# Optimization experiments

Hardware: AMD Instinct MI355X
Metric: run time of the kernel (lower is better)

## Reference

```python
import jax, jax.numpy as jnp
import numpy as np
from functools import partial

B, S, D_IN, H = 8, 2048, 1024, 1024
V = 50257
NUM_CODEWORDS, EMB_DIM = 256, 16
NUM_NEURONS, TOP_K = 64, 16  # top_k = sparsity(0.25) * 64
TILE_ROWS = 16
NUM_TILES = H // TILE_ROWS  # 64 -> decoder out_features = 1024
FREQS = (1.0, 2.0, 4.0)
MAX_LEN = 1024


def setup_inputs() -> dict:
    key = jax.random.key(0)
    ks = jax.random.split(key, 16)
    s = 0.02
    return {
        "inputs": jax.random.normal(ks[0], (B, S, D_IN), jnp.float32),
        "Wt": jax.random.normal(ks[1], (H, D_IN), jnp.float32) * s,
        "bt": jnp.zeros((H,), jnp.float32),
        "Wq": jax.random.normal(ks[2], (H, H), jnp.float32) * s,
        "bq": jnp.zeros((H,), jnp.float32),
        "Wk": jax.random.normal(ks[3], (H, H), jnp.float32) * s,
        "bk": jnp.zeros((H,), jnp.float32),
        "Wv": jax.random.normal(ks[4], (H, H), jnp.float32) * s,
        "bv": jnp.zeros((H,), jnp.float32),
        "Wo": jax.random.normal(ks[5], (D_IN, H), jnp.float32) * s,
        "bo": jnp.zeros((D_IN,), jnp.float32),
        "codebook": jax.random.normal(ks[6], (NUM_CODEWORDS, EMB_DIM), jnp.float32) * s,
        "instructions": jax.random.randint(ks[7], (NUM_TILES * TILE_ROWS, D_IN // EMB_DIM), 0, NUM_CODEWORDS),
        "W_lm": jax.random.normal(ks[8], (V, NUM_TILES * TILE_ROWS), jnp.float32) * s,
        "b_lm": jnp.zeros((V,), jnp.float32),
    }


def _positional_bias(seq_len):
    # AttentionBasisSynthesizer: sin/cos atoms at freqs (1,2,4), gains=1, shifts=0
    ang = 2.0 * jnp.pi * jnp.arange(seq_len, dtype=jnp.float32) / MAX_LEN
    bias = jnp.zeros((seq_len,), jnp.float32)
    for f in FREQS:
        bias = bias + jnp.sin(f * ang) + jnp.cos(f * ang)
    return bias  # [S]


def _forward(inputs, Wt, bt, Wq, bq, Wk, bk, Wv, bv, Wo, bo, codebook, instructions, W_lm, b_lm):
    tokens = inputs @ Wt.T + bt                       # [B,S,H]
    q = tokens @ Wq.T + bq
    k = tokens @ Wk.T + bk
    v = tokens @ Wv.T + bv
    # per-step KV-cache loop == causal attention over prefix; vectorize
    scores = jnp.einsum("bqh,bkh->bqk", q, k) / jnp.sqrt(jnp.float32(H))
    scores = scores + _positional_bias(S)[None, None, :]
    i = jnp.arange(S)
    causal = i[:, None] >= i[None, :]                 # [S,S]
    scores = jnp.where(causal[None], scores, -jnp.inf)
    attn = jnp.einsum("bqk,bkh->bqh", jax.nn.softmax(scores, axis=-1), v)  # [B,S,H]
    # sparse routing: group into NUM_NEURONS neurons, keep top-k by L2 norm,
    # softmax weights over kept neurons, straight-through combine with dense path
    g = attn.reshape(B, S, NUM_NEURONS, H // NUM_NEURONS)
    sc = jnp.sqrt(jnp.sum(g * g, axis=-1))            # [B,S,N]
    vals, idx = jax.lax.top_k(sc, TOP_K)              # [B,S,K]
    w = jax.nn.softmax(vals, axis=-1)
    onehot = jax.nn.one_hot(idx, NUM_NEURONS, dtype=attn.dtype)  # [B,S,K,N]
    wfull = jnp.einsum("bsk,bskn->bsn", w, onehot)    # [B,S,N]
    combined = (g * wfull[..., None]).reshape(B, S, H)
    combined = combined + (attn - jax.lax.stop_gradient(attn))  # straight-through
    dec_in = combined @ Wo.T + bo                     # [B,S,D_IN]
    x = jnp.mean(dec_in, axis=1)                      # [B,D_IN]
    # DemopackDecoder: weight rows assembled from codebook via instruction indices
    W_dec = codebook[instructions].reshape(NUM_TILES * TILE_ROWS, D_IN)
    hidden = x @ W_dec.T                              # [B, 1024]
    return hidden @ W_lm.T + b_lm                     # [B, V]


def reference(inputs, Wt, bt, Wq, bq, Wk, bk, Wv, bv, Wo, bo, codebook, instructions, W_lm, b_lm):
    return _forward(inputs, Wt, bt, Wq, bq, Wk, bk, Wv, bv, Wo, bo, codebook, instructions, W_lm, b_lm)
```

## Files before the change

### kernel.cpp

```cpp
#include <hip/hip_runtime.h>
#include <cstdint>
#include <cstddef>

#define B_   8
#define S_   2048
#define DIN_ 1024
#define H_   1024
#define V_   50257

typedef unsigned short ushort_t;
typedef __bf16 bf16x8 __attribute__((ext_vector_type(8)));
typedef float  f32x4  __attribute__((ext_vector_type(4)));

__device__ __forceinline__ ushort_t f2bf(float x) {
    unsigned u = __float_as_uint(x);
    u = (u + 0x7fffu + ((u >> 16) & 1u)) >> 16;
    return (ushort_t)u;
}

__device__ __forceinline__ void async16(const void* g, void* s) {
    __builtin_amdgcn_global_load_lds(
        (const __attribute__((address_space(1))) unsigned int*)g,
        (__attribute__((address_space(3))) unsigned int*)s, 16, 0, 0);
}

__device__ __forceinline__ float wredmax(float v) {
#pragma unroll
    for (int o = 32; o; o >>= 1) v = fmaxf(v, __shfl_xor(v, o));
    return v;
}
__device__ __forceinline__ float wredsum(float v) {
#pragma unroll
    for (int o = 32; o; o >>= 1) v += __shfl_xor(v, o);
    return v;
}

__global__ void f2bf_vec(const float* __restrict__ in, ushort_t* __restrict__ out, int n4) {
    int i = blockIdx.x * 256 + threadIdx.x;
    if (i >= n4) return;
    float4 f = ((const float4*)in)[i];
    ushort4 u;
    u.x = f2bf(f.x); u.y = f2bf(f.y); u.z = f2bf(f.z); u.w = f2bf(f.w);
    ((ushort4*)out)[i] = u;
}

__global__ void f2bf_w3(const float* __restrict__ Wq, const float* __restrict__ Wk,
                        const float* __restrict__ Wv, ushort_t* __restrict__ out) {
    int i = blockIdx.x * 256 + threadIdx.x;
    int w = i >> 18, off = i & 262143;
    const float* src = w == 0 ? Wq : (w == 1 ? Wk : Wv);
    float4 f = ((const float4*)src)[off];
    ushort4 u;
    u.x = f2bf(f.x); u.y = f2bf(f.y); u.z = f2bf(f.z); u.w = f2bf(f.w);
    ((ushort4*)(out + (size_t)w * 1048576))[off] = u;
}

__global__ void pos_bias_kernel(float* __restrict__ bias) {
    int k = blockIdx.x * 256 + threadIdx.x;
    if (k >= S_) return;
    float ang = 6.283185307179586f * (float)k / 1024.0f;
    float b = 0.f;
    b += sinf(1.f * ang) + cosf(1.f * ang);
    b += sinf(2.f * ang) + cosf(2.f * ang);
    b += sinf(4.f * ang) + cosf(4.f * ang);
    bias[k] = b;
}

__global__ __launch_bounds__(256)
void transpose_wt(const float* __restrict__ Wt, ushort_t* __restrict__ wtT) {
    __shared__ float t[64][65];
    int k0 = blockIdx.x * 64, i0 = blockIdx.y * 64;
    int tx = threadIdx.x & 63, ty = threadIdx.x >> 6;
#pragma unroll
    for (int j = 0; j < 16; j++) {
        int k = ty * 16 + j;
        t[k][tx] = Wt[(size_t)(k0 + k) * DIN_ + i0 + tx];
    }
    __syncthreads();
#pragma unroll
    for (int j = 0; j < 16; j++) {
        int i = ty * 16 + j;
        wtT[(size_t)(i0 + i) * H_ + k0 + tx] = f2bf(t[tx][i]);
    }
}

__global__ __launch_bounds__(256)
void bcomb_kernel(const float* __restrict__ Wq, const float* __restrict__ Wk,
                  const float* __restrict__ Wv, const float* __restrict__ bq,
                  const float* __restrict__ bk, const float* __restrict__ bv,
                  const float* __restrict__ bt, float* __restrict__ bcomb) {
    int wave = threadIdx.x >> 6, lane = threadIdx.x & 63;
    int j = blockIdx.x * 4 + wave;
    const float* W  = j < 1024 ? Wq : (j < 2048 ? Wk : Wv);
    const float* bb = j < 1024 ? bq : (j < 2048 ? bk : bv);
    int rowj = j & 1023;
    const float4* wr4 = (const float4*)(W + (size_t)rowj * 1024);
    const float4* bt4 = (const float4*)bt;
    float s = 0.f;
#pragma unroll
    for (int c = 0; c < 4; c++) {
        float4 w = wr4[c * 64 + lane];
        float4 b = bt4[c * 64 + lane];
        s += w.x * b.x + w.y * b.y + w.z * b.z + w.w * b.w;
    }
    s = wredsum(s);
    if (lane == 0) bcomb[j] = s + bb[rowj];
}

template <int OUT_BF16>
__global__ __launch_bounds__(256)
void gemm_bt(const ushort_t* __restrict__ A, int lda,
             const ushort_t* __restrict__ Bt, int ldb,
             void* __restrict__ Cv, int ldc, int K, const float* __restrict__ bias) {
    int bn = blockIdx.x, bm = blockIdx.y;
    __shared__ ushort_t As[128 * 32];
    __shared__ ushort_t Bs[128 * 32];
    int tid = threadIdx.x, wave = tid >> 6, lane = tid & 63;
    int wr = wave >> 1, wc = wave & 1;
    int nkt = K >> 5;
    int srow = lane >> 2, scol = (lane & 3) * 8;
    size_t arow0 = (size_t)bm * 128, brow0 = (size_t)bn * 128;
    f32x4 acc[4][4];
#pragma unroll
    for (int m = 0; m < 4; m++)
#pragma unroll
        for (int n = 0; n < 4; n++) acc[m][n] = f32x4{0.f, 0.f, 0.f, 0.f};
    for (int kt = 0; kt < nkt; ++kt) {
        int k0 = kt * 32;
#pragma unroll
        for (int i = 0; i < 2; i++) {
            int reg = wave * 2 + i;
            int row = reg * 16 + srow;
            async16(A + (arow0 + row) * (size_t)lda + k0 + scol, (ushort_t*)As + reg * 512);
            async16(Bt + (brow0 + row) * (size_t)ldb + k0 + scol, (ushort_t*)Bs + reg * 512);
        }
        __syncthreads();
        bf16x8 af[4], bfr[4];
#pragma unroll
        for (int m = 0; m < 4; m++)
            af[m] = *(const bf16x8*)&As[(wr * 64 + m * 16 + (lane & 15)) * 32 + (lane >> 4) * 8];
#pragma unroll
        for (int n = 0; n < 4; n++)
            bfr[n] = *(const bf16x8*)&Bs[(wc * 64 + n * 16 + (lane & 15)) * 32 + (lane >> 4) * 8];
#pragma unroll
        for (int m = 0; m < 4; m++)
#pragma unroll
            for (int n = 0; n < 4; n++)
                acc[m][n] = __builtin_amdgcn_mfma_f32_16x16x32_bf16(af[m], bfr[n], acc[m][n], 0, 0, 0);
        __syncthreads();
    }
    int rl = (lane >> 4) * 4, cl = lane & 15;
#pragma unroll
    for (int m = 0; m < 4; m++)
#pragma unroll
        for (int n = 0; n < 4; n++) {
            int col = bn * 128 + wc * 64 + n * 16 + cl;
            float badd = bias ? bias[col] : 0.f;
#pragma unroll
            for (int r = 0; r < 4; r++) {
                int row = bm * 128 + wr * 64 + m * 16 + rl + r;
                float v = acc[m][n][r] + badd;
                size_t off = (size_t)row * ldc + col;
                if (OUT_BF16) ((ushort_t*)Cv)[off] = f2bf(v);
                else          ((float*)Cv)[off] = v;
            }
        }
}

template <int OUT_BF16, int MODE>
__global__ __launch_bounds__(512, 2)
void gemm256(const ushort_t* __restrict__ A, size_t sAb, int lda,
             const ushort_t* __restrict__ Bt, size_t sBb, int ldb,
             void* __restrict__ Cv, size_t sCb, int ldc,
             int K, const float* __restrict__ bias, int nbn, int nwg,
             float* __restrict__ Cv2) {
    extern __shared__ char lds[];
    int bz = blockIdx.y;
    int bm, bn, koff = 0, nkt;
    void* Cuse = Cv;
    size_t sCuse = sCb;
    if (MODE == 2) {
        int x = blockIdx.x;
        if (x < 32) {
            bm = x >> 2; bn = x & 3;
            int km = (bm + 1) * 256; if (km > 1024) km = 1024;
            nkt = km >> 6;
        } else {
            int j = x - 32;
            bm = 7 - (j >> 2); bn = j & 3;
            koff = 1024;
            nkt = ((bm + 1) * 256 - 1024) >> 6;
            Cuse = Cv2;
            sCuse = (size_t)1024 * 1024;
        }
    } else {
        int orig = blockIdx.x;
        int qq = nwg >> 3, rr8 = nwg & 7;
        int xcd = orig & 7, bidx = orig >> 3;
        int wgid = (xcd < rr8 ? xcd * (qq + 1) : rr8 * (qq + 1) + (xcd - rr8) * qq) + bidx;
        if (MODE == 1) {
            int w = wgid;
            bm = 0;
            while ((bm + 1) * (bm + 2) / 2 <= w) bm++;
            bn = w - bm * (bm + 1) / 2;
        } else {
            bm = wgid / nbn; bn = wgid - bm * nbn;
        }
        nkt = K >> 6;
    }

    const ushort_t* Ab = A + (size_t)bz * sAb;
    const ushort_t* Bb = Bt + (size_t)bz * sBb;
    int tid = threadIdx.x, wave = tid >> 6, lane = tid & 63;
    int wr = wave >> 2, wc = wave & 3;

    int srow = wave * 8 + (lane >> 3);
    int sswz = ((lane & 7) ^ (lane >> 3)) * 8;
    const ushort_t* Ag = Ab + ((size_t)bm * 256 + srow) * (size_t)lda + sswz + koff;
    const ushort_t* Bg = Bb + ((size_t)bn * 256 + srow) * (size_t)ldb + sswz + koff;
    int sdst = wave * 1024;

    int fr = lane & 15, g = lane >> 4;
    int kx = (fr >> 2) & 1;
    int gsw = (g ^ (fr & 3)) * 16;
    int aoff = wr * 16384 + fr * 128 + gsw;
    int boff = 32768 + (wc >> 1) * 16384 + ((wc & 1) * 64 + fr) * 128 + gsw;
    int ks0 = kx << 6, ks1 = (kx ^ 1) << 6;

    f32x4 acc[8][4];
#pragma unroll
    for (int m = 0; m < 8; m++)
#pragma unroll
        for (int n = 0; n < 4; n++) acc[m][n] = f32x4{0.f, 0.f, 0.f, 0.f};

#define STG_A(t, h, bo)                                                        \
    do {                                                                       \
        async16(Ag + (size_t)((h) * 128) * lda + (t) * 64,                     \
                lds + (bo) + (h) * 16384 + sdst);                              \
        async16(Ag + (size_t)((h) * 128 + 64) * lda + (t) * 64,                \
                lds + (bo) + (h) * 16384 + 8192 + sdst);                       \
    } while (0)
#define STG_B(t, h, bo)                                                        \
    do {                                                                       \
        async16(Bg + (size_t)((h) * 128) * ldb + (t) * 64,                     \
                lds + (bo) + 32768 + (h) * 16384 + sdst);                      \
        async16(Bg + (size_t)((h) * 128 + 64) * ldb + (t) * 64,                \
                lds + (bo) + 32768 + (h) * 16384 + 8192 + sdst);               \
    } while (0)

    STG_A(0, 0, 0); STG_A(0, 1, 0); STG_B(0, 0, 0); STG_B(0, 1, 0);
    STG_A(1, 0, 65536); STG_A(1, 1, 65536); STG_B(1, 0, 65536); STG_B(1, 1, 65536);
    asm volatile("s_waitcnt vmcnt(8)" ::: "memory");
    __builtin_amdgcn_sched_barrier(0);
    __builtin_amdgcn_s_barrier();
    __builtin_amdgcn_sched_barrier(0);

    bf16x8 af03[4][2], af47[4][2], bf01[2][2], bf23[2][2];
#pragma unroll
    for (int mf = 0; mf < 4; mf++) {
        af03[mf][0] = *(const bf16x8*)(lds + aoff + mf * 2048 + ks0);
        af03[mf][1] = *(const bf16x8*)(lds + aoff + mf * 2048 + ks1);
    }
#pragma unroll
    for (int nf = 0; nf < 2; nf++) {
        bf01[nf][0] = *(const bf16x8*)(lds + boff + nf * 2048 + ks0);
        bf01[nf][1] = *(const bf16x8*)(lds + boff + nf * 2048 + ks1);
    }

    int bufo = 0;
    for (int t = 0; t < nkt; ++t, bufo ^= 65536) {
        int nb = bufo ^ 65536;
#pragma unroll
        for (int mf = 0; mf < 4; mf++) {
            af47[mf][0] = *(const bf16x8*)(lds + bufo + aoff + (mf + 4) * 2048 + ks0);
            af47[mf][1] = *(const bf16x8*)(lds + bufo + aoff + (mf + 4) * 2048 + ks1);
        }
#pragma unroll
        for (int nf = 0; nf < 2; nf++) {
            bf23[nf][0] = *(const bf16x8*)(lds + bufo + boff + (nf + 2) * 2048 + ks0);
            bf23[nf][1] = *(const bf16x8*)(lds + bufo + boff + (nf + 2) * 2048 + ks1);
        }
        __builtin_amdgcn_s_setprio(1);
#pragma unroll
        for (int mf = 0; mf < 4; mf++)
#pragma unroll
            for (int nf = 0; nf < 2; nf++) {
                acc[mf][nf] = __builtin_amdgcn_mfma_f32_16x16x32_bf16(af03[mf][0], bf01[nf][0], acc[mf][nf], 0, 0, 0);
                acc[mf][nf] = __builtin_amdgcn_mfma_f32_16x16x32_bf16(af03[mf][1], bf01[nf][1], acc[mf][nf], 0, 0, 0);
            }
        __builtin_amdgcn_s_setprio(0);
        __builtin_amdgcn_sched_barrier(0);
        asm volatile("s_waitcnt lgkmcnt(0)" ::: "memory");
        __builtin_amdgcn_sched_barrier(0);
        __builtin_amdgcn_s_barrier();
        __builtin_amdgcn_sched_barrier(0);

        __builtin_amdgcn_s_setprio(1);
#pragma unroll
        for (int mf = 0; mf < 4; mf++)
#pragma unroll
            for (int nf = 0; nf < 2; nf++) {
                acc[mf + 4][nf] = __builtin_amdgcn_mfma_f32_16x16x32_bf16(af47[mf][0], bf01[nf][0], acc[mf + 4][nf], 0, 0, 0);
                acc[mf + 4][nf] = __builtin_amdgcn_mfma_f32_16x16x32_bf16(af47[mf][1], bf01[nf][1], acc[mf + 4][nf], 0, 0, 0);
            }
        __builtin_amdgcn_s_setprio(0);
        __builtin_amdgcn_sched_barrier(0);
        __builtin_amdgcn_s_barrier();
        __builtin_amdgcn_sched_barrier(0);

        if (t + 2 < nkt) STG_A(t + 2, 0, bufo);
        __builtin_amdgcn_s_setprio(1);
#pragma unroll
        for (int mf = 0; mf < 4; mf++)
#pragma unroll
            for (int nf = 0; nf < 2; nf++) {
                acc[mf][nf + 2] = __builtin_amdgcn_mfma_f32_16x16x32_bf16(af03[mf][0], bf23[nf][0], acc[mf][nf + 2], 0, 0, 0);
                acc[mf][nf + 2] = __builtin_amdgcn_mfma_f32_16x16x32_bf16(af03[mf][1], bf23[nf][1], acc[mf][nf + 2], 0, 0, 0);
            }
        __builtin_amdgcn_s_setprio(0);
        __builtin_amdgcn_sched_barrier(0);
        if (t + 1 < nkt) {
            if (t + 2 < nkt) { asm volatile("s_waitcnt vmcnt(2)" ::: "memory"); }
            else             { asm volatile("s_waitcnt vmcnt(0)" ::: "memory"); }
        }
        __builtin_amdgcn_s_barrier();
        __builtin_amdgcn_sched_barrier(0);

        if (t + 1 < nkt) {
#pragma unroll
            for (int mf = 0; mf < 4; mf++) {
                af03[mf][0] = *(const bf16x8*)(lds + nb + aoff + mf * 2048 + ks0);
                af03[mf][1] = *(const bf16x8*)(lds + nb + aoff + mf * 2048 + ks1);
            }
#pragma unroll
            for (int nf = 0; nf < 2; nf++) {
                bf01[nf][0] = *(const bf16x8*)(lds + nb + boff + nf * 2048 + ks0);
                bf01[nf][1] = *(const bf16x8*)(lds + nb + boff + nf * 2048 + ks1);
            }
        }
        if (t + 2 < nkt) { STG_A(t + 2, 1, bufo); STG_B(t + 2, 0, bufo); STG_B(t + 2, 1, bufo); }
        __builtin_amdgcn_s_setprio(1);
#pragma unroll
        for (int mf = 0; mf < 4; mf++)
#pragma unroll
            for (int nf = 0; nf < 2; nf++) {
                acc[mf + 4][nf + 2] = __builtin_amdgcn_mfma_f32_16x16x32_bf16(af47[mf][0], bf23[nf][0], acc[mf + 4][nf + 2], 0, 0, 0);
                acc[mf + 4][nf + 2] = __builtin_amdgcn_mfma_f32_16x16x32_bf16(af47[mf][1], bf23[nf][1], acc[mf + 4][nf + 2], 0, 0, 0);
            }
        __builtin_amdgcn_s_setprio(0);
        __builtin_amdgcn_sched_barrier(0);
        __builtin_amdgcn_s_barrier();
        __builtin_amdgcn_sched_barrier(0);
    }
#undef STG_A
#undef STG_B

    int rl = (lane >> 4) * 4, cl = lane & 15;
#pragma unroll
    for (int mf = 0; mf < 8; mf++)
#pragma unroll
        for (int nf = 0; nf < 4; nf++) {
            int col = bn * 256 + wc * 64 + nf * 16 + cl;
            float badd = bias ? bias[col] : 0.f;
#pragma unroll
            for (int r = 0; r < 4; r++) {
                int row = bm * 256 + wr * 128 + mf * 16 + rl + r;
                float v = acc[mf][nf][r] + badd;
                size_t off = (size_t)bz * sCuse + (size_t)row * ldc + col;
                if (OUT_BF16) ((ushort_t*)Cuse)[off] = f2bf(v);
                else          ((float*)Cuse)[off] = v;
            }
        }
}

__global__ __launch_bounds__(256)
void transpose_v(const ushort_t* __restrict__ qkv, ushort_t* __restrict__ vT) {
    __shared__ ushort_t t[64][66];
    int b = blockIdx.z;
    int s0 = blockIdx.x * 64, h0 = blockIdx.y * 64;
    int tx = threadIdx.x & 63, ty = threadIdx.x >> 6;
#pragma unroll
    for (int i = 0; i < 16; i++) {
        int s = ty * 16 + i;
        t[s][tx] = qkv[((size_t)b * S_ + s0 + s) * 3072 + 2048 + h0 + tx];
    }
    __syncthreads();
#pragma unroll
    for (int i = 0; i < 16; i++) {
        int h = ty * 16 + i;
        vT[((size_t)b * H_ + h0 + h) * S_ + s0 + tx] = t[tx][h];
    }
}

__global__ __launch_bounds__(256)
void softmax_kernel(const float* __restrict__ scores, ushort_t* __restrict__ P,
                    const float* __restrict__ bias) {
    __shared__ float srs[S_];
    __shared__ float red[8];
    int q = blockIdx.x, b = blockIdx.y;
    int L = q + 1;
    int tid = threadIdx.x;
    const float* srow = scores + ((size_t)b * S_ + q) * S_;
    const float scale = 0.03125f;

    float lm = -3e38f;
    for (int k = tid; k < L; k += 256) {
        float s = srow[k] * scale + bias[k];
        srs[k] = s;
        lm = fmaxf(lm, s);
    }
    lm = wredmax(lm);
    if ((tid & 63) == 0) red[tid >> 6] = lm;
    __syncthreads();
    float m = fmaxf(fmaxf(red[0], red[1]), fmaxf(red[2], red[3]));

    float ls = 0.f;
    for (int k = tid; k < L; k += 256) {
        float e = __expf(srs[k] - m);
        srs[k] = e;
        ls += e;
    }
    ls = wredsum(ls);
    if ((tid & 63) == 0) red[4 + (tid >> 6)] = ls;
    __syncthreads();
    float invs = 1.f / (red[4] + red[5] + red[6] + red[7]);

    int kz = ((q >> 8) + 1) * 256;
    ushort_t* prow = P + ((size_t)b * S_ + q) * S_;
    for (int k = tid; k < kz; k += 256)
        prow[k] = (k < L) ? f2bf(srs[k] * invs) : (ushort_t)0;
}

__global__ __launch_bounds__(256)
void routing_kernel(const float* __restrict__ attn, const float* __restrict__ attn2,
                    ushort_t* __restrict__ combined) {
    int wave = threadIdx.x >> 6, lane = threadIdx.x & 63;
    size_t row = (size_t)blockIdx.x * 4 + wave;
    const float4* a4 = (const float4*)(attn + row * H_);
    float4 x0 = a4[lane * 4 + 0], x1 = a4[lane * 4 + 1];
    float4 x2 = a4[lane * 4 + 2], x3 = a4[lane * 4 + 3];
    int q = (int)(row & 2047);
    if (q >= 1024) {
        size_t b = row >> 11;
        const float4* a2 = (const float4*)(attn2 + ((b * 1024 + (size_t)(q - 1024)) * H_));
        float4 y0 = a2[lane * 4 + 0], y1 = a2[lane * 4 + 1];
        float4 y2 = a2[lane * 4 + 2], y3 = a2[lane * 4 + 3];
        x0.x += y0.x; x0.y += y0.y; x0.z += y0.z; x0.w += y0.w;
        x1.x += y1.x; x1.y += y1.y; x1.z += y1.z; x1.w += y1.w;
        x2.x += y2.x; x2.y += y2.y; x2.z += y2.z; x2.w += y2.w;
        x3.x += y3.x; x3.y += y3.y; x3.z += y3.z; x3.w += y3.w;
    }
    float ss = x0.x * x0.x + x0.y * x0.y + x0.z * x0.z + x0.w * x0.w
             + x1.x * x1.x + x1.y * x1.y + x1.z * x1.z + x1.w * x1.w
             + x2.x * x2.x + x2.y * x2.y + x2.z * x2.z + x2.w * x2.w
             + x3.x * x3.x + x3.y * x3.y + x3.z * x3.z + x3.w * x3.w;
    float sc = sqrtf(ss);

    float v = sc, thr = 0.f, mx = 0.f;
#pragma unroll
    for (int i = 0; i < 16; i++) {
        float mm = wredmax(v);
        if (i == 0) mx = mm;
        thr = mm;
        if (v == mm) v = -1e30f;
    }
    float e = (sc >= thr) ? __expf(sc - mx) : 0.f;
    float se = wredsum(e);
    float w = e / se;

    const float xs[16] = {x0.x, x0.y, x0.z, x0.w, x1.x, x1.y, x1.z, x1.w,
                          x2.x, x2.y, x2.z, x2.w, x3.x, x3.y, x3.z, x3.w};
    union { ushort_t u[16]; uint4 q4[2]; } pk;
#pragma unroll
    for (int j = 0; j < 16; j++) pk.u[j] = f2bf(xs[j] * w);
    uint4* dst = (uint4*)(combined + row * H_ + lane * 16);
    dst[0] = pk.q4[0];
    dst[1] = pk.q4[1];
}

__global__ void cmean_part(const ushort_t* __restrict__ comb, float* __restrict__ part) {
    int d = blockIdx.x * 256 + threadIdx.x;
    int sc = blockIdx.y, b = blockIdx.z;
    const ushort_t* p = comb + ((size_t)b * S_ + sc * 128) * H_ + d;
    float s = 0.f;
    for (int i = 0; i < 128; i++) s += __uint_as_float((unsigned)p[(size_t)i * H_] << 16);
    part[((size_t)b * 16 + sc) * H_ + d] = s;
}

__global__ void cmean_final(const float* __restrict__ part, float* __restrict__ cm) {
    int idx = blockIdx.x * 256 + threadIdx.x;
    int b = idx >> 10, d = idx & 1023;
    float s = 0.f;
#pragma unroll
    for (int c = 0; c < 16; c++) s += part[((size_t)b * 16 + c) * DIN_ + d];
    cm[idx] = s * (1.0f / 2048.0f);
}

__global__ __launch_bounds__(256)
void xgemv(const float* __restrict__ cm, const float* __restrict__ Wo,
           const float* __restrict__ bo, float* __restrict__ x) {
    int wave = threadIdx.x >> 6, lane = threadIdx.x & 63;
    int i = blockIdx.x * 4 + wave;
    const float4* wr4 = (const float4*)(Wo + (size_t)i * H_);
    float4 w[4];
#pragma unroll
    for (int c = 0; c < 4; c++) w[c] = wr4[c * 64 + lane];
    float accv[B_];
#pragma unroll
    for (int b = 0; b < B_; b++) {
        const float4* c4 = (const float4*)(cm + (size_t)b * H_);
        float s = 0.f;
#pragma unroll
        for (int c = 0; c < 4; c++) {
            float4 h = c4[c * 64 + lane];
            s += w[c].x * h.x + w[c].y * h.y + w[c].z * h.z + w[c].w * h.w;
        }
        accv[b] = wredsum(s);
    }
    if (lane == 0) {
        float bi = bo[i];
#pragma unroll
        for (int b = 0; b < B_; b++) x[(size_t)b * DIN_ + i] = accv[b] + bi;
    }
}

__global__ __launch_bounds__(64)
void decode_hidden(const float* __restrict__ x, const float* __restrict__ codebook,
                   const int* __restrict__ instr, float* __restrict__ hidden) {
    int r = blockIdx.x;
    int lane = threadIdx.x;
    int idx = instr[r * 64 + lane];
    const float4* cw = (const float4*)(codebook + (size_t)idx * 16);
    float4 c0 = cw[0], c1 = cw[1], c2 = cw[2], c3 = cw[3];
    float acc[B_];
#pragma unroll
    for (int b = 0; b < B_; b++) {
        const float4* xb = (const float4*)(x + (size_t)b * DIN_ + lane * 16);
        float4 h0 = xb[0], h1 = xb[1], h2 = xb[2], h3 = xb[3];
        acc[b] = c0.x * h0.x + c0.y * h0.y + c0.z * h0.z + c0.w * h0.w
               + c1.x * h1.x + c1.y * h1.y + c1.z * h1.z + c1.w * h1.w
               + c2.x * h2.x + c2.y * h2.y + c2.z * h2.z + c2.w * h2.w
               + c3.x * h3.x + c3.y * h3.y + c3.z * h3.z + c3.w * h3.w;
    }
#pragma unroll
    for (int b = 0; b < B_; b++) acc[b] = wredsum(acc[b]);
    if (lane == 0) {
#pragma unroll
        for (int b = 0; b < B_; b++) hidden[(size_t)b * 1024 + r] = acc[b];
    }
}

__global__ __launch_bounds__(256)
void lm_head(const float* __restrict__ Wlm, const float* __restrict__ hidden,
             const float* __restrict__ blm, float* __restrict__ out) {
    int wave = threadIdx.x >> 6, lane = threadIdx.x & 63;
    for (int v = blockIdx.x * 4 + wave; v < V_; v += gridDim.x * 4) {
        const float4* wrow = (const float4*)(Wlm + (size_t)v * 1024);
        float acc[B_];
#pragma unroll
        for (int b = 0; b < B_; b++) acc[b] = 0.f;
#pragma unroll
        for (int rr = 0; rr < 4; rr++) {
            float4 wv = wrow[rr * 64 + lane];
#pragma unroll
            for (int b = 0; b < B_; b++) {
                float4 hv = ((const float4*)hidden)[b * 256 + rr * 64 + lane];
                acc[b] += wv.x * hv.x + wv.y * hv.y + wv.z * hv.z + wv.w * hv.w;
            }
        }
#pragma unroll
        for (int b = 0; b < B_; b++) acc[b] = wredsum(acc[b]);
        if (lane == 0) {
            float bl = blm[v];
#pragma unroll
            for (int b = 0; b < B_; b++) out[(size_t)b * V_ + v] = acc[b] + bl;
        }
    }
}

extern "C" void kernel_launch(void* const* d_in, const int* in_sizes, int n_in,
                              void* d_out, int out_size, void* d_ws, size_t ws_size,
                              hipStream_t stream) {
    const float* inputs = (const float*)d_in[0];
    const float* Wt  = (const float*)d_in[1];
    const float* bt  = (const float*)d_in[2];
    const float* Wq  = (const float*)d_in[3];
    const float* bq  = (const float*)d_in[4];
    const float* Wk  = (const float*)d_in[5];
    const float* bk  = (const float*)d_in[6];
    const float* Wv  = (const float*)d_in[7];
    const float* bv  = (const float*)d_in[8];
    const float* Wo  = (const float*)d_in[9];
    const float* bo  = (const float*)d_in[10];
    const float* codebook = (const float*)d_in[11];
    const int*   instructions = (const int*)d_in[12];
    const float* Wlm = (const float*)d_in[13];
    const float* blm = (const float*)d_in[14];
    float* out = (float*)d_out;

    (void)hipFuncSetAttribute(reinterpret_cast<const void*>(&gemm256<1, 0>),
                              hipFuncAttributeMaxDynamicSharedMemorySize, 131072);
    (void)hipFuncSetAttribute(reinterpret_cast<const void*>(&gemm256<0, 1>),
                              hipFuncAttributeMaxDynamicSharedMemorySize, 131072);
    (void)hipFuncSetAttribute(reinterpret_cast<const void*>(&gemm256<0, 2>),
                              hipFuncAttributeMaxDynamicSharedMemorySize, 131072);

    const size_t MB = 1024 * 1024;
    char* ws = (char*)d_ws;
    ushort_t* wqkv_bf = (ushort_t*)(ws + 0);
    ushort_t* wtT_bf  = (ushort_t*)(ws + 6 * MB);
    ushort_t* wcomb   = (ushort_t*)(ws + 8 * MB);
    float* bcomb  = (float*)(ws + 14 * MB);
    float* pbias  = (float*)(ws + 14 * MB + 64 * 1024);
    float* cm     = (float*)(ws + 14 * MB + 128 * 1024);
    float* xbuf   = (float*)(ws + 14 * MB + 192 * 1024);
    float* hidden = (float*)(ws + 14 * MB + 256 * 1024);
    float* part   = (float*)(ws + 14 * MB + 512 * 1024);
    ushort_t* inbf   = (ushort_t*)(ws + 16 * MB);
    ushort_t* qkv    = (ushort_t*)(ws + 48 * MB);
    ushort_t* vT     = (ushort_t*)(ws + 144 * MB);
    float* scores    = (float*)(ws + 176 * MB);
    ushort_t* P      = (ushort_t*)(ws + 304 * MB);
    float* attn      = (float*)(ws + 48 * MB);
    float* attn2     = (float*)(ws + 112 * MB);
    ushort_t* combined = (ushort_t*)(ws + 176 * MB);

    f2bf_vec<<<16384, 256, 0, stream>>>(inputs, inbf, 4194304);
    f2bf_w3<<<3072, 256, 0, stream>>>(Wq, Wk, Wv, wqkv_bf);
    transpose_wt<<<dim3(16, 16), 256, 0, stream>>>(Wt, wtT_bf);
    bcomb_kernel<<<768, 256, 0, stream>>>(Wq, Wk, Wv, bq, bk, bv, bt, bcomb);
    pos_bias_kernel<<<8, 256, 0, stream>>>(pbias);

    gemm_bt<1><<<dim3(8, 24), 256, 0, stream>>>(wqkv_bf, 1024, wtT_bf, 1024,
                                                wcomb, 1024, 1024, nullptr);

    gemm256<1, 0><<<dim3(768, 1), 512, 131072, stream>>>(
        inbf, 0, 1024, wcomb, 0, 1024, qkv, 0, 3072, 1024, bcomb, 12, 768, nullptr);

    transpose_v<<<dim3(32, 16, 8), 256, 0, stream>>>(qkv, vT);

    gemm256<0, 1><<<dim3(36, 8), 512, 131072, stream>>>(
        qkv, (size_t)S_ * 3072, 3072, qkv + 1024, (size_t)S_ * 3072, 3072,
        scores, (size_t)S_ * S_, S_, 1024, nullptr, 36, 36, nullptr);

    softmax_kernel<<<dim3(S_, B_), 256, 0, stream>>>(scores, P, pbias);

    gemm256<0, 2><<<dim3(48, 8), 512, 131072, stream>>>(
        P, (size_t)S_ * S_, S_, vT, (size_t)H_ * S_, S_,
        attn, (size_t)S_ * H_, H_, S_, nullptr, 0, 0, attn2 - (size_t)1024 * 1024);

    routing_kernel<<<4096, 256, 0, stream>>>(attn, attn2, combined);

    cmean_part<<<dim3(4, 16, 8), 256, 0, stream>>>(combined, part);
    cmean_final<<<32, 256, 0, stream>>>(part, cm);
    xgemv<<<256, 256, 0, stream>>>(cm, Wo, bo, xbuf);

    decode_hidden<<<1024, 64, 0, stream>>>(xbuf, codebook, instructions, hidden);

    lm_head<<<2048, 256, 0, stream>>>(Wlm, hidden, blm, out);
}
```

Baseline: 458.2 us.

## Restructure GEMM main loop into 8-phase ping-pong schedule with interleaved staging

```diff
diff --git a/kernel.cpp b/kernel.cpp
--- a/kernel.cpp
+++ b/kernel.cpp
@@ -247,113 +247,96 @@
         async16(Bg + (size_t)((h) * 128 + 64) * ldb + (t) * 64,                \
                 lds + (bo) + 32768 + (h) * 16384 + 8192 + sdst);               \
     } while (0)
+#define RD_A(DST, BUF, MOFS)                                                   \
+    _Pragma("unroll")                                                          \
+    for (int mf = 0; mf < 4; mf++) {                                           \
+        DST[mf][0] = *(const bf16x8*)(lds + (BUF) + aoff + (mf + (MOFS)) * 2048 + ks0); \
+        DST[mf][1] = *(const bf16x8*)(lds + (BUF) + aoff + (mf + (MOFS)) * 2048 + ks1); \
+    }
+#define RD_B(DST, BUF, NOFS)                                                   \
+    _Pragma("unroll")                                                          \
+    for (int nf = 0; nf < 2; nf++) {                                           \
+        DST[nf][0] = *(const bf16x8*)(lds + (BUF) + boff + (nf + (NOFS)) * 2048 + ks0); \
+        DST[nf][1] = *(const bf16x8*)(lds + (BUF) + boff + (nf + (NOFS)) * 2048 + ks1); \
+    }
+#define MMQ(AF, BF, MO, NO)                                                    \
+    _Pragma("unroll")                                                          \
+    for (int mf = 0; mf < 4; mf++)                                             \
+        _Pragma("unroll")                                                      \
+        for (int nf = 0; nf < 2; nf++) {                                       \
+            acc[mf + (MO)][nf + (NO)] = __builtin_amdgcn_mfma_f32_16x16x32_bf16(AF[mf][0], BF[nf][0], acc[mf + (MO)][nf + (NO)], 0, 0, 0); \
+            acc[mf + (MO)][nf + (NO)] = __builtin_amdgcn_mfma_f32_16x16x32_bf16(AF[mf][1], BF[nf][1], acc[mf + (MO)][nf + (NO)], 0, 0, 0); \
+        }
+#define SB __builtin_amdgcn_sched_barrier(0)
+#define PH_PRE                                                                 \
+    SB; __builtin_amdgcn_s_barrier();                                          \
+    asm volatile("s_waitcnt lgkmcnt(0)" ::: "memory");                         \
+    SB; __builtin_amdgcn_s_setprio(1)
+#define PH_POST                                                                \
+    __builtin_amdgcn_s_setprio(0); SB; __builtin_amdgcn_s_barrier(); SB
 
     STG_A(0, 0, 0); STG_A(0, 1, 0); STG_B(0, 0, 0); STG_B(0, 1, 0);
-    STG_A(1, 0, 65536); STG_A(1, 1, 65536); STG_B(1, 0, 65536); STG_B(1, 1, 65536);
-    asm volatile("s_waitcnt vmcnt(8)" ::: "memory");
-    __builtin_amdgcn_sched_barrier(0);
-    __builtin_amdgcn_s_barrier();
-    __builtin_amdgcn_sched_barrier(0);
-
-    bf16x8 af03[4][2], af47[4][2], bf01[2][2], bf23[2][2];
-#pragma unroll
-    for (int mf = 0; mf < 4; mf++) {
-        af03[mf][0] = *(const bf16x8*)(lds + aoff + mf * 2048 + ks0);
-        af03[mf][1] = *(const bf16x8*)(lds + aoff + mf * 2048 + ks1);
-    }
-#pragma unroll
-    for (int nf = 0; nf < 2; nf++) {
-        bf01[nf][0] = *(const bf16x8*)(lds + boff + nf * 2048 + ks0);
-        bf01[nf][1] = *(const bf16x8*)(lds + boff + nf * 2048 + ks1);
-    }
-
-    int bufo = 0;
-    for (int t = 0; t < nkt; ++t, bufo ^= 65536) {
-        int nb = bufo ^ 65536;
-#pragma unroll
-        for (int mf = 0; mf < 4; mf++) {
-            af47[mf][0] = *(const bf16x8*)(lds + bufo + aoff + (mf + 4) * 2048 + ks0);
-            af47[mf][1] = *(const bf16x8*)(lds + bufo + aoff + (mf + 4) * 2048 + ks1);
-        }
-#pragma unroll
-        for (int nf = 0; nf < 2; nf++) {
-            bf23[nf][0] = *(const bf16x8*)(lds + bufo + boff + (nf + 2) * 2048 + ks0);
-            bf23[nf][1] = *(const bf16x8*)(lds + bufo + boff + (nf + 2) * 2048 + ks1);
-        }
+    STG_A(1, 0, 65536); STG_A(1, 1, 65536);
+    asm volatile("s_waitcnt vmcnt(4)" ::: "memory");
+    SB; __builtin_amdgcn_s_barrier(); SB;
+
+    bf16x8 a03[4][2], a47[4][2], b01[2][2], b23[2][2];
+
+    int niter = nkt >> 1;
+    for (int i = 0; i < niter; ++i) {
+        int u = 2 * i;
+        bool lastp = (u + 2 >= nkt);
+
+        RD_A(a03, 0, 0); RD_B(b01, 0, 0);
+        STG_B(u + 1, 0, 65536);
+        PH_PRE; MMQ(a03, b01, 0, 0); PH_POST;
+
+        RD_A(a47, 0, 4);
+        STG_B(u + 1, 1, 65536);
+        PH_PRE; MMQ(a47, b01, 4, 0); PH_POST;
+
+        RD_B(b23, 0, 2);
+        if (!lastp) STG_A(u + 2, 0, 0);
+        PH_PRE; MMQ(a03, b23, 0, 2); PH_POST;
+
+        if (!lastp) STG_A(u + 2, 1, 0);
+        SB;
+        if (!lastp) { asm volatile("s_waitcnt vmcnt(4)" ::: "memory"); }
+        else        { asm volatile("s_waitcnt vmcnt(0)" ::: "memory"); }
+        SB; __builtin_amdgcn_s_barrier(); SB;
         __builtin_amdgcn_s_setprio(1);
-#pragma unroll
-        for (int mf = 0; mf < 4; mf++)
-#pragma unroll
-            for (int nf = 0; nf < 2; nf++) {
-                acc[mf][nf] = __builtin_amdgcn_mfma_f32_16x16x32_bf16(af03[mf][0], bf01[nf][0], acc[mf][nf], 0, 0, 0);
-                acc[mf][nf] = __builtin_amdgcn_mfma_f32_16x16x32_bf16(af03[mf][1], bf01[nf][1], acc[mf][nf], 0, 0, 0);
-            }
-        __builtin_amdgcn_s_setprio(0);
-        __builtin_amdgcn_sched_barrier(0);
-        asm volatile("s_waitcnt lgkmcnt(0)" ::: "memory");
-        __builtin_amdgcn_sched_barrier(0);
-        __builtin_amdgcn_s_barrier();
-        __builtin_amdgcn_sched_barrier(0);
-
+        MMQ(a47, b23, 4, 2);
+        PH_POST;
+
+        RD_A(a03, 65536, 0); RD_B(b01, 65536, 0);
+        if (!lastp) STG_B(u + 2, 0, 0);
+        PH_PRE; MMQ(a03, b01, 0, 0); PH_POST;
+
+        RD_A(a47, 65536, 4);
+        if (!lastp) STG_B(u + 2, 1, 0);
+        PH_PRE; MMQ(a47, b01, 4, 0); PH_POST;
+
+        RD_B(b23, 65536, 2);
+        if (!lastp) STG_A(u + 3, 0, 65536);
+        PH_PRE; MMQ(a03, b23, 0, 2); PH_POST;
+
+        if (!lastp) STG_A(u + 3, 1, 65536);
+        SB;
+        if (!lastp) { asm volatile("s_waitcnt vmcnt(4)" ::: "memory"); }
+        else        { asm volatile("s_waitcnt vmcnt(0)" ::: "memory"); }
+        SB; __builtin_amdgcn_s_barrier(); SB;
         __builtin_amdgcn_s_setprio(1);
-#pragma unroll
-        for (int mf = 0; mf < 4; mf++)
-#pragma unroll
-            for (int nf = 0; nf < 2; nf++) {
-                acc[mf + 4][nf] = __builtin_amdgcn_mfma_f32_16x16x32_bf16(af47[mf][0], bf01[nf][0], acc[mf + 4][nf], 0, 0, 0);
-                acc[mf + 4][nf] = __builtin_amdgcn_mfma_f32_16x16x32_bf16(af47[mf][1], bf01[nf][1], acc[mf + 4][nf], 0, 0, 0);
-            }
-        __builtin_amdgcn_s_setprio(0);
-        __builtin_amdgcn_sched_barrier(0);
-        __builtin_amdgcn_s_barrier();
-        __builtin_amdgcn_sched_barrier(0);
-
-        if (t + 2 < nkt) STG_A(t + 2, 0, bufo);
-        __builtin_amdgcn_s_setprio(1);
-#pragma unroll
-        for (int mf = 0; mf < 4; mf++)
-#pragma unroll
-            for (int nf = 0; nf < 2; nf++) {
-                acc[mf][nf + 2] = __builtin_amdgcn_mfma_f32_16x16x32_bf16(af03[mf][0], bf23[nf][0], acc[mf][nf + 2], 0, 0, 0);
-                acc[mf][nf + 2] = __builtin_amdgcn_mfma_f32_16x16x32_bf16(af03[mf][1], bf23[nf][1], acc[mf][nf + 2], 0, 0, 0);
-            }
-        __builtin_amdgcn_s_setprio(0);
-        __builtin_amdgcn_sched_barrier(0);
-        if (t + 1 < nkt) {
-            if (t + 2 < nkt) { asm volatile("s_waitcnt vmcnt(2)" ::: "memory"); }
-            else             { asm volatile("s_waitcnt vmcnt(0)" ::: "memory"); }
-        }
-        __builtin_amdgcn_s_barrier();
-        __builtin_amdgcn_sched_barrier(0);
-
-        if (t + 1 < nkt) {
-#pragma unroll
-            for (int mf = 0; mf < 4; mf++) {
-                af03[mf][0] = *(const bf16x8*)(lds + nb + aoff + mf * 2048 + ks0);
-                af03[mf][1] = *(const bf16x8*)(lds + nb + aoff + mf * 2048 + ks1);
-            }
-#pragma unroll
-            for (int nf = 0; nf < 2; nf++) {
-                bf01[nf][0] = *(const bf16x8*)(lds + nb + boff + nf * 2048 + ks0);
-                bf01[nf][1] = *(const bf16x8*)(lds + nb + boff + nf * 2048 + ks1);
-            }
-        }
-        if (t + 2 < nkt) { STG_A(t + 2, 1, bufo); STG_B(t + 2, 0, bufo); STG_B(t + 2, 1, bufo); }
-        __builtin_amdgcn_s_setprio(1);
-#pragma unroll
-        for (int mf = 0; mf < 4; mf++)
-#pragma unroll
-            for (int nf = 0; nf < 2; nf++) {
-                acc[mf + 4][nf + 2] = __builtin_amdgcn_mfma_f32_16x16x32_bf16(af47[mf][0], bf23[nf][0], acc[mf + 4][nf + 2], 0, 0, 0);
-                acc[mf + 4][nf + 2] = __builtin_amdgcn_mfma_f32_16x16x32_bf16(af47[mf][1], bf23[nf][1], acc[mf + 4][nf + 2], 0, 0, 0);
-            }
-        __builtin_amdgcn_s_setprio(0);
-        __builtin_amdgcn_sched_barrier(0);
-        __builtin_amdgcn_s_barrier();
-        __builtin_amdgcn_sched_barrier(0);
+        MMQ(a47, b23, 4, 2);
+        PH_POST;
     }
 #undef STG_A
 #undef STG_B
+#undef RD_A
+#undef RD_B
+#undef MMQ
+#undef SB
+#undef PH_PRE
+#undef PH_POST
 
     int rl = (lane >> 4) * 4, cl = lane & 15;
 #pragma unroll
```

After: 535.4 us. 16.8% more time.
